# Kernel tuning notes

Measured on AMD Instinct MI355X. Metric: run time of the kernel, lower is better.

The kernel has to match this reference:

```python
import jax, jax.numpy as jnp
import numpy as np

SEQLEN = (512, 1024, 2048, 1536, 768, 1280, 896, 640)
HEAD_NUM = 16
HIDDEN = 1024  # head_size = 64


def setup_inputs() -> dict:
    key = jax.random.key(0)
    k1, k2 = jax.random.split(key)
    total_a = HEAD_NUM * sum(s * s for s in SEQLEN)  # packed per-seq (H, s, s) blocks
    a = jax.random.normal(k1, (total_a,), dtype=jnp.float32) * 0.02
    b = jax.random.normal(k2, (sum(SEQLEN), HIDDEN), dtype=jnp.float32)
    return {"a": a, "b": b, "seqlen": list(SEQLEN), "head_num": HEAD_NUM}


def reference(a, b, seqlen, head_num):
    """Ragged strided bmm2: per sequence i, per head h:
    C_i[:, h*hs:(h+1)*hs] = A_i[h] @ B_i[:, h*hs:(h+1)*hs].
    a packed flat as sum_i (head_num, s_i, s_i); b is (sum(s), hidden).
    """
    hidden = b.shape[1]
    hs = hidden // head_num
    outs = []
    a_off = 0
    t_off = 0
    for s in seqlen:  # static loop over ragged batch (lengths are compile-time)
        ai = jax.lax.dynamic_slice(a, (a_off,), (head_num * s * s,)).reshape(head_num, s, s)
        bi = jax.lax.dynamic_slice(b, (t_off, 0), (s, hidden)).reshape(s, head_num, hs)
        # (H, q, k) x (k, H, d) -> (q, H, d) -> (q, hidden)
        ci = jnp.einsum('hqk,khd->qhd', ai, bi).reshape(s, hidden)
        outs.append(ci)
        a_off += head_num * s * s
        t_off += s
    return jnp.concatenate(outs, axis=0)  # (sum(seqlen), hidden)
```

## Files before the change

### kernel.cpp

```cpp
#include <hip/hip_runtime.h>
#include <hip/hip_bf16.h>

typedef __attribute__((ext_vector_type(4))) float f32x4;
typedef __attribute__((ext_vector_type(8))) short bf16x8;

__device__ inline unsigned short f2b(float f) {
    union { float f; unsigned u; } v; v.f = f;
    unsigned r = v.u + 0x7FFF + ((v.u >> 16) & 1);
    return (unsigned short)(r >> 16);
}
__device__ inline unsigned pack2(float lo, float hi) {
    return (unsigned)f2b(lo) | ((unsigned)f2b(hi) << 16);
}

#define LDB 40

__global__ __launch_bounds__(256) void bmm2_kernel(const float* __restrict__ a,
                                                   const float* __restrict__ b,
                                                   float* __restrict__ out) {
    const int  cumblk[9] = {0,64,192,448,640,736,896,1008,1088};
    const int  slen[8]   = {512,1024,2048,1536,768,1280,896,640};
    const long aoff[8]   = {0,4194304,20971520,88080384,125829120,135266304,161480704,174325760};
    const int  toff[8]   = {0,512,1536,3584,5120,5888,7168,8064};

    __shared__ unsigned short Bt[64 * LDB];

    int bid = blockIdx.x;
    int i = 0;
    #pragma unroll
    for (int t = 0; t < 7; ++t) if (bid >= cumblk[t + 1]) i = t + 1;

    int rem  = bid - cumblk[i];
    int s    = slen[i];
    int nmb  = s >> 7;
    int head = rem / nmb;
    int mb   = rem - head * nmb;

    const float* A  = a + aoff[i] + (long)head * s * s + (long)mb * 128 * s;
    const float* Bp = b + (long)toff[i] * 1024 + head * 64;
    float*       Cp = out + (long)(toff[i] + mb * 128) * 1024 + head * 64;

    int tid  = threadIdx.x;
    int lane = tid & 63;
    int wave = tid >> 6;
    int lrow = lane & 15;
    int lgrp = lane >> 4;

    f32x4 acc[2][4] = {};

    int k2 = tid >> 4;
    int j0 = (tid & 15) * 4;

    const float* arow0 = A + (long)(wave * 32 + lrow) * s + lgrp * 8;
    const float* arow1 = arow0 + (long)16 * s;

    for (int k0 = 0; k0 < s; k0 += 32) {
        f32x4 a00 = *(const f32x4*)(arow0 + k0);
        f32x4 a01 = *(const f32x4*)(arow0 + k0 + 4);
        f32x4 a10 = *(const f32x4*)(arow1 + k0);
        f32x4 a11 = *(const f32x4*)(arow1 + k0 + 4);

        const float* bp = Bp + (long)(k0 + 2 * k2) * 1024 + j0;
        f32x4 b0 = *(const f32x4*)bp;
        f32x4 b1 = *(const f32x4*)(bp + 1024);

        __syncthreads();
        #pragma unroll
        for (int e = 0; e < 4; ++e)
            *(unsigned*)&Bt[(j0 + e) * LDB + 2 * k2] = pack2(b0[e], b1[e]);
        __syncthreads();

        bf16x8 bf[4];
        #pragma unroll
        for (int nt = 0; nt < 4; ++nt)
            bf[nt] = *(const bf16x8*)&Bt[(nt * 16 + lrow) * LDB + lgrp * 8];

        bf16x8 af0, af1;
        #pragma unroll
        for (int e = 0; e < 4; ++e) {
            af0[e]     = (short)f2b(a00[e]);
            af0[e + 4] = (short)f2b(a01[e]);
            af1[e]     = (short)f2b(a10[e]);
            af1[e + 4] = (short)f2b(a11[e]);
        }

        #pragma unroll
        for (int nt = 0; nt < 4; ++nt) {
            acc[0][nt] = __builtin_amdgcn_mfma_f32_16x16x32_bf16(af0, bf[nt], acc[0][nt], 0, 0, 0);
            acc[1][nt] = __builtin_amdgcn_mfma_f32_16x16x32_bf16(af1, bf[nt], acc[1][nt], 0, 0, 0);
        }
    }

    #pragma unroll
    for (int mt = 0; mt < 2; ++mt)
        #pragma unroll
        for (int nt = 0; nt < 4; ++nt)
            #pragma unroll
            for (int r = 0; r < 4; ++r) {
                int q = wave * 32 + mt * 16 + lgrp * 4 + r;
                Cp[(long)q * 1024 + nt * 16 + lrow] = acc[mt][nt][r];
            }
}

extern "C" void kernel_launch(void* const* d_in, const int* in_sizes, int n_in,
                              void* d_out, int out_size, void* d_ws, size_t ws_size,
                              hipStream_t stream) {
    const float* a = (const float*)d_in[0];
    const float* b = (const float*)d_in[1];
    float* out = (float*)d_out;
    bmm2_kernel<<<1088, 256, 0, stream>>>(a, b, out);
}
```

Measured before the change: 181.3 us.

## Pre-transpose B to bf16 in workspace and drop LDS staging in bmm2

```diff
diff --git a/kernel.cpp b/kernel.cpp
--- a/kernel.cpp
+++ b/kernel.cpp
@@ -4,90 +4,116 @@
 typedef __attribute__((ext_vector_type(4))) float f32x4;
 typedef __attribute__((ext_vector_type(8))) short bf16x8;
 
-__device__ inline unsigned short f2b(float f) {
+__device__ inline short f2b(float f) {
     union { float f; unsigned u; } v; v.f = f;
     unsigned r = v.u + 0x7FFF + ((v.u >> 16) & 1);
-    return (unsigned short)(r >> 16);
+    return (short)(r >> 16);
 }
 __device__ inline unsigned pack2(float lo, float hi) {
-    return (unsigned)f2b(lo) | ((unsigned)f2b(hi) << 16);
-}
-
-#define LDB 40
-
-__global__ __launch_bounds__(256) void bmm2_kernel(const float* __restrict__ a,
-                                                   const float* __restrict__ b,
-                                                   float* __restrict__ out) {
-    const int  cumblk[9] = {0,64,192,448,640,736,896,1008,1088};
-    const int  slen[8]   = {512,1024,2048,1536,768,1280,896,640};
-    const long aoff[8]   = {0,4194304,20971520,88080384,125829120,135266304,161480704,174325760};
-    const int  toff[8]   = {0,512,1536,3584,5120,5888,7168,8064};
-
-    __shared__ unsigned short Bt[64 * LDB];
+    return (unsigned)(unsigned short)f2b(lo) | ((unsigned)(unsigned short)f2b(hi) << 16);
+}
+
+__global__ __launch_bounds__(256) void transposeB(const float* __restrict__ b,
+                                                  unsigned short* __restrict__ bt) {
+    const int cumtb[9] = {0,128,384,896,1280,1472,1792,2016,2176};
+    const int slen[8]  = {512,1024,2048,1536,768,1280,896,640};
+    const int toff[8]  = {0,512,1536,3584,5120,5888,7168,8064};
+    __shared__ unsigned short T[64][72];
 
     int bid = blockIdx.x;
     int i = 0;
     #pragma unroll
+    for (int t = 0; t < 7; ++t) if (bid >= cumtb[t + 1]) i = t + 1;
+    int rem  = bid - cumtb[i];
+    int s    = slen[i];
+    int nkt  = s >> 6;
+    int head = rem / nkt;
+    int t0   = (rem - head * nkt) << 6;
+
+    int tid = threadIdx.x;
+    int row = tid >> 2, cg = tid & 3;
+    const float* src = b + (long)(toff[i] + t0 + row) * 1024 + head * 64 + cg * 16;
+    #pragma unroll
+    for (int e4 = 0; e4 < 4; ++e4) {
+        f32x4 v = *(const f32x4*)(src + e4 * 4);
+        #pragma unroll
+        for (int e = 0; e < 4; ++e)
+            T[cg * 16 + e4 * 4 + e][row] = (unsigned short)f2b(v[e]);
+    }
+    __syncthreads();
+    int col = tid >> 2, kq = tid & 3;
+    unsigned short* dst = bt + (long)toff[i] * 1024 + (long)head * 64 * s
+                             + (long)col * s + t0 + kq * 16;
+    *(bf16x8*)dst       = *(const bf16x8*)&T[col][kq * 16];
+    *(bf16x8*)(dst + 8) = *(const bf16x8*)&T[col][kq * 16 + 8];
+}
+
+__global__ __launch_bounds__(256) void bmm2_main(const float* __restrict__ a,
+                                                 const unsigned short* __restrict__ bt,
+                                                 float* __restrict__ out) {
+    const int  cumblk[9] = {0,256,448,608,736,848,944,1024,1088};
+    const int  slen[8]   = {2048,1536,1280,1024,896,768,640,512};
+    const long aoff[8]   = {20971520,88080384,135266304,4194304,161480704,125829120,174325760,0};
+    const int  toff[8]   = {1536,3584,5888,512,7168,5120,8064,0};
+
+    int bid = blockIdx.x;
+    int i = 0;
+    #pragma unroll
     for (int t = 0; t < 7; ++t) if (bid >= cumblk[t + 1]) i = t + 1;
-
     int rem  = bid - cumblk[i];
     int s    = slen[i];
     int nmb  = s >> 7;
     int head = rem / nmb;
     int mb   = rem - head * nmb;
 
-    const float* A  = a + aoff[i] + (long)head * s * s + (long)mb * 128 * s;
-    const float* Bp = b + (long)toff[i] * 1024 + head * 64;
-    float*       Cp = out + (long)(toff[i] + mb * 128) * 1024 + head * 64;
-
-    int tid  = threadIdx.x;
-    int lane = tid & 63;
-    int wave = tid >> 6;
-    int lrow = lane & 15;
-    int lgrp = lane >> 4;
+    const float* A = a + aoff[i] + (long)head * s * s + (long)mb * 128 * s;
+    const unsigned short* Bt = bt + (long)toff[i] * 1024 + (long)head * 64 * s;
+    float* Cp = out + (long)(toff[i] + mb * 128) * 1024 + head * 64;
+
+    int tid = threadIdx.x, lane = tid & 63, wave = tid >> 6;
+    int lrow = lane & 15, lgrp = lane >> 4;
+
+    const float* ar0 = A + (long)(wave * 32 + lrow) * s + lgrp * 8;
+    const float* ar1 = ar0 + (long)16 * s;
+    const unsigned short* bp = Bt + (long)lrow * s + lgrp * 8;
 
     f32x4 acc[2][4] = {};
 
-    int k2 = tid >> 4;
-    int j0 = (tid & 15) * 4;
-
-    const float* arow0 = A + (long)(wave * 32 + lrow) * s + lgrp * 8;
-    const float* arow1 = arow0 + (long)16 * s;
-
-    for (int k0 = 0; k0 < s; k0 += 32) {
-        f32x4 a00 = *(const f32x4*)(arow0 + k0);
-        f32x4 a01 = *(const f32x4*)(arow0 + k0 + 4);
-        f32x4 a10 = *(const f32x4*)(arow1 + k0);
-        f32x4 a11 = *(const f32x4*)(arow1 + k0 + 4);
-
-        const float* bp = Bp + (long)(k0 + 2 * k2) * 1024 + j0;
-        f32x4 b0 = *(const f32x4*)bp;
-        f32x4 b1 = *(const f32x4*)(bp + 1024);
-
-        __syncthreads();
-        #pragma unroll
-        for (int e = 0; e < 4; ++e)
-            *(unsigned*)&Bt[(j0 + e) * LDB + 2 * k2] = pack2(b0[e], b1[e]);
-        __syncthreads();
-
-        bf16x8 bf[4];
-        #pragma unroll
-        for (int nt = 0; nt < 4; ++nt)
-            bf[nt] = *(const bf16x8*)&Bt[(nt * 16 + lrow) * LDB + lgrp * 8];
-
-        bf16x8 af0, af1;
+    for (int k0 = 0; k0 < s; k0 += 64) {
+        f32x4 a00 = *(const f32x4*)(ar0 + k0);
+        f32x4 a01 = *(const f32x4*)(ar0 + k0 + 4);
+        f32x4 a10 = *(const f32x4*)(ar1 + k0);
+        f32x4 a11 = *(const f32x4*)(ar1 + k0 + 4);
+        f32x4 a02 = *(const f32x4*)(ar0 + k0 + 32);
+        f32x4 a03 = *(const f32x4*)(ar0 + k0 + 36);
+        f32x4 a12 = *(const f32x4*)(ar1 + k0 + 32);
+        f32x4 a13 = *(const f32x4*)(ar1 + k0 + 36);
+
+        bf16x8 bf0[4], bf1[4];
+        #pragma unroll
+        for (int nt = 0; nt < 4; ++nt) {
+            bf0[nt] = *(const bf16x8*)(bp + (long)nt * 16 * s + k0);
+            bf1[nt] = *(const bf16x8*)(bp + (long)nt * 16 * s + k0 + 32);
+        }
+
+        bf16x8 af0, af1, af2, af3;
         #pragma unroll
         for (int e = 0; e < 4; ++e) {
-            af0[e]     = (short)f2b(a00[e]);
-            af0[e + 4] = (short)f2b(a01[e]);
-            af1[e]     = (short)f2b(a10[e]);
-            af1[e + 4] = (short)f2b(a11[e]);
-        }
-
-        #pragma unroll
-        for (int nt = 0; nt < 4; ++nt) {
-            acc[0][nt] = __builtin_amdgcn_mfma_f32_16x16x32_bf16(af0, bf[nt], acc[0][nt], 0, 0, 0);
-            acc[1][nt] = __builtin_amdgcn_mfma_f32_16x16x32_bf16(af1, bf[nt], acc[1][nt], 0, 0, 0);
+            af0[e] = f2b(a00[e]); af0[e + 4] = f2b(a01[e]);
+            af1[e] = f2b(a10[e]); af1[e + 4] = f2b(a11[e]);
+            af2[e] = f2b(a02[e]); af2[e + 4] = f2b(a03[e]);
+            af3[e] = f2b(a12[e]); af3[e + 4] = f2b(a13[e]);
+        }
+
+        #pragma unroll
+        for (int nt = 0; nt < 4; ++nt) {
+            acc[0][nt] = __builtin_amdgcn_mfma_f32_16x16x32_bf16(af0, bf0[nt], acc[0][nt], 0, 0, 0);
+            acc[1][nt] = __builtin_amdgcn_mfma_f32_16x16x32_bf16(af1, bf0[nt], acc[1][nt], 0, 0, 0);
+        }
+        #pragma unroll
+        for (int nt = 0; nt < 4; ++nt) {
+            acc[0][nt] = __builtin_amdgcn_mfma_f32_16x16x32_bf16(af2, bf1[nt], acc[0][nt], 0, 0, 0);
+            acc[1][nt] = __builtin_amdgcn_mfma_f32_16x16x32_bf16(af3, bf1[nt], acc[1][nt], 0, 0, 0);
         }
     }
 
@@ -102,11 +128,89 @@
             }
 }
 
+#define LDB 40
+__global__ __launch_bounds__(256) void bmm2_kernel_lds(const float* __restrict__ a,
+                                                       const float* __restrict__ b,
+                                                       float* __restrict__ out) {
+    const int  cumblk[9] = {0,64,192,448,640,736,896,1008,1088};
+    const int  slen[8]   = {512,1024,2048,1536,768,1280,896,640};
+    const long aoff[8]   = {0,4194304,20971520,88080384,125829120,135266304,161480704,174325760};
+    const int  toff[8]   = {0,512,1536,3584,5120,5888,7168,8064};
+    __shared__ unsigned short Bt[64 * LDB];
+
+    int bid = blockIdx.x;
+    int i = 0;
+    #pragma unroll
+    for (int t = 0; t < 7; ++t) if (bid >= cumblk[t + 1]) i = t + 1;
+    int rem = bid - cumblk[i];
+    int s = slen[i];
+    int nmb = s >> 7;
+    int head = rem / nmb;
+    int mb = rem - head * nmb;
+
+    const float* A  = a + aoff[i] + (long)head * s * s + (long)mb * 128 * s;
+    const float* Bp = b + (long)toff[i] * 1024 + head * 64;
+    float*       Cp = out + (long)(toff[i] + mb * 128) * 1024 + head * 64;
+
+    int tid = threadIdx.x, lane = tid & 63, wave = tid >> 6;
+    int lrow = lane & 15, lgrp = lane >> 4;
+    f32x4 acc[2][4] = {};
+    int k2 = tid >> 4;
+    int j0 = (tid & 15) * 4;
+    const float* arow0 = A + (long)(wave * 32 + lrow) * s + lgrp * 8;
+    const float* arow1 = arow0 + (long)16 * s;
+
+    for (int k0 = 0; k0 < s; k0 += 32) {
+        f32x4 a00 = *(const f32x4*)(arow0 + k0);
+        f32x4 a01 = *(const f32x4*)(arow0 + k0 + 4);
+        f32x4 a10 = *(const f32x4*)(arow1 + k0);
+        f32x4 a11 = *(const f32x4*)(arow1 + k0 + 4);
+        const float* bpp = Bp + (long)(k0 + 2 * k2) * 1024 + j0;
+        f32x4 b0 = *(const f32x4*)bpp;
+        f32x4 b1 = *(const f32x4*)(bpp + 1024);
+        __syncthreads();
+        #pragma unroll
+        for (int e = 0; e < 4; ++e)
+            *(unsigned*)&Bt[(j0 + e) * LDB + 2 * k2] = pack2(b0[e], b1[e]);
+        __syncthreads();
+        bf16x8 bf[4];
+        #pragma unroll
+        for (int nt = 0; nt < 4; ++nt)
+            bf[nt] = *(const bf16x8*)&Bt[(nt * 16 + lrow) * LDB + lgrp * 8];
+        bf16x8 af0, af1;
+        #pragma unroll
+        for (int e = 0; e < 4; ++e) {
+            af0[e] = f2b(a00[e]); af0[e + 4] = f2b(a01[e]);
+            af1[e] = f2b(a10[e]); af1[e + 4] = f2b(a11[e]);
+        }
+        #pragma unroll
+        for (int nt = 0; nt < 4; ++nt) {
+            acc[0][nt] = __builtin_amdgcn_mfma_f32_16x16x32_bf16(af0, bf[nt], acc[0][nt], 0, 0, 0);
+            acc[1][nt] = __builtin_amdgcn_mfma_f32_16x16x32_bf16(af1, bf[nt], acc[1][nt], 0, 0, 0);
+        }
+    }
+    #pragma unroll
+    for (int mt = 0; mt < 2; ++mt)
+        #pragma unroll
+        for (int nt = 0; nt < 4; ++nt)
+            #pragma unroll
+            for (int r = 0; r < 4; ++r) {
+                int q = wave * 32 + mt * 16 + lgrp * 4 + r;
+                Cp[(long)q * 1024 + nt * 16 + lrow] = acc[mt][nt][r];
+            }
+}
+
 extern "C" void kernel_launch(void* const* d_in, const int* in_sizes, int n_in,
                               void* d_out, int out_size, void* d_ws, size_t ws_size,
                               hipStream_t stream) {
     const float* a = (const float*)d_in[0];
     const float* b = (const float*)d_in[1];
     float* out = (float*)d_out;
-    bmm2_kernel<<<1088, 256, 0, stream>>>(a, b, out);
-}
+    const size_t BT_BYTES = 8704UL * 1024UL * 2UL;
+    if (ws_size >= BT_BYTES) {
+        transposeB<<<2176, 256, 0, stream>>>(b, (unsigned short*)d_ws);
+        bmm2_main<<<1088, 256, 0, stream>>>(a, (const unsigned short*)d_ws, out);
+    } else {
+        bmm2_kernel_lds<<<1088, 256, 0, stream>>>(a, b, out);
+    }
+}
```

Result: slower. 228.9 us (+26.2%).

## Double-buffer B tile with 64-wide K steps, smaller blocks, longest-first scheduling

Applied to the files above, without the earlier changes.

```diff
diff --git a/kernel.cpp b/kernel.cpp
--- a/kernel.cpp
+++ b/kernel.cpp
@@ -4,101 +4,131 @@
 typedef __attribute__((ext_vector_type(4))) float f32x4;
 typedef __attribute__((ext_vector_type(8))) short bf16x8;
 
-__device__ inline unsigned short f2b(float f) {
-    union { float f; unsigned u; } v; v.f = f;
-    unsigned r = v.u + 0x7FFF + ((v.u >> 16) & 1);
-    return (unsigned short)(r >> 16);
+__device__ __forceinline__ unsigned cvt2(float lo, float hi) {
+    float2 t; t.x = lo; t.y = hi;
+    __hip_bfloat162 h = __float22bfloat162_rn(t);
+    union { __hip_bfloat162 h; unsigned u; } c; c.h = h; return c.u;
 }
-__device__ inline unsigned pack2(float lo, float hi) {
-    return (unsigned)f2b(lo) | ((unsigned)f2b(hi) << 16);
+__device__ __forceinline__ bf16x8 cvt8(f32x4 lo, f32x4 hi) {
+    union { bf16x8 v; unsigned u[4]; } r;
+    r.u[0] = cvt2(lo[0], lo[1]); r.u[1] = cvt2(lo[2], lo[3]);
+    r.u[2] = cvt2(hi[0], hi[1]); r.u[3] = cvt2(hi[2], hi[3]);
+    return r.v;
 }
 
-#define LDB 40
+__global__ __launch_bounds__(128, 4) void bmm2_k(const float* __restrict__ a,
+                                                 const float* __restrict__ b,
+                                                 float* __restrict__ out) {
+    const int  cumblk[9] = {0,512,896,1216,1472,1696,1888,2048,2176};
+    const int  slen[8]   = {2048,1536,1280,1024,896,768,640,512};
+    const long aoff[8]   = {20971520,88080384,135266304,4194304,161480704,125829120,174325760,0};
+    const int  toff[8]   = {1536,3584,5888,512,7168,5120,8064,0};
 
-__global__ __launch_bounds__(256) void bmm2_kernel(const float* __restrict__ a,
-                                                   const float* __restrict__ b,
-                                                   float* __restrict__ out) {
-    const int  cumblk[9] = {0,64,192,448,640,736,896,1008,1088};
-    const int  slen[8]   = {512,1024,2048,1536,768,1280,896,640};
-    const long aoff[8]   = {0,4194304,20971520,88080384,125829120,135266304,161480704,174325760};
-    const int  toff[8]   = {0,512,1536,3584,5120,5888,7168,8064};
-
-    __shared__ unsigned short Bt[64 * LDB];
+    __shared__ unsigned short Bt[2][64 * 72];
 
     int bid = blockIdx.x;
     int i = 0;
     #pragma unroll
     for (int t = 0; t < 7; ++t) if (bid >= cumblk[t + 1]) i = t + 1;
-
     int rem  = bid - cumblk[i];
     int s    = slen[i];
-    int nmb  = s >> 7;
+    int nmb  = s >> 6;
     int head = rem / nmb;
     int mb   = rem - head * nmb;
 
-    const float* A  = a + aoff[i] + (long)head * s * s + (long)mb * 128 * s;
+    const float* A  = a + aoff[i] + (long)head * s * s + (long)mb * 64 * s;
     const float* Bp = b + (long)toff[i] * 1024 + head * 64;
-    float*       Cp = out + (long)(toff[i] + mb * 128) * 1024 + head * 64;
+    float*       Cp = out + (long)(toff[i] + mb * 64) * 1024 + head * 64;
 
-    int tid  = threadIdx.x;
-    int lane = tid & 63;
-    int wave = tid >> 6;
-    int lrow = lane & 15;
-    int lgrp = lane >> 4;
+    int tid = threadIdx.x, lane = tid & 63, wave = tid >> 6;
+    int lrow = lane & 15, lgrp = lane >> 4;
+
+    int j0 = (tid & 15) * 4;
+    int kb = (tid >> 4) * 8;
+    const float* bsrc = Bp + (long)kb * 1024 + j0;
+
+    const float* ar0 = A + (long)(wave * 32 + lrow) * s + lgrp * 8;
+    const float* ar1 = ar0 + (long)16 * s;
 
     f32x4 acc[2][4] = {};
+    int NT = s >> 6;
 
-    int k2 = tid >> 4;
-    int j0 = (tid & 15) * 4;
+    {
+        f32x4 r[8];
+        #pragma unroll
+        for (int q = 0; q < 8; ++q) r[q] = *(const f32x4*)(bsrc + (long)q * 1024);
+        #pragma unroll
+        for (int e = 0; e < 4; ++e) {
+            uint4 w;
+            w.x = cvt2(r[0][e], r[1][e]); w.y = cvt2(r[2][e], r[3][e]);
+            w.z = cvt2(r[4][e], r[5][e]); w.w = cvt2(r[6][e], r[7][e]);
+            *(uint4*)&Bt[0][(j0 + e) * 72 + kb] = w;
+        }
+    }
+    __syncthreads();
 
-    const float* arow0 = A + (long)(wave * 32 + lrow) * s + lgrp * 8;
-    const float* arow1 = arow0 + (long)16 * s;
+    for (int t = 0; t < NT; ++t) {
+        int cur = t & 1, nxt = cur ^ 1;
+        int k0 = t << 6;
+        int kn = (t + 1 < NT) ? (k0 + 64) : 0;
 
-    for (int k0 = 0; k0 < s; k0 += 32) {
-        f32x4 a00 = *(const f32x4*)(arow0 + k0);
-        f32x4 a01 = *(const f32x4*)(arow0 + k0 + 4);
-        f32x4 a10 = *(const f32x4*)(arow1 + k0);
-        f32x4 a11 = *(const f32x4*)(arow1 + k0 + 4);
-
-        const float* bp = Bp + (long)(k0 + 2 * k2) * 1024 + j0;
-        f32x4 b0 = *(const f32x4*)bp;
-        f32x4 b1 = *(const f32x4*)(bp + 1024);
+        f32x4 r[8];
+        #pragma unroll
+        for (int q = 0; q < 8; ++q) r[q] = *(const f32x4*)(bsrc + (long)(kn + q) * 1024);
 
         __syncthreads();
-        #pragma unroll
-        for (int e = 0; e < 4; ++e)
-            *(unsigned*)&Bt[(j0 + e) * LDB + 2 * k2] = pack2(b0[e], b1[e]);
-        __syncthreads();
 
-        bf16x8 bf[4];
-        #pragma unroll
-        for (int nt = 0; nt < 4; ++nt)
-            bf[nt] = *(const bf16x8*)&Bt[(nt * 16 + lrow) * LDB + lgrp * 8];
-
-        bf16x8 af0, af1;
         #pragma unroll
         for (int e = 0; e < 4; ++e) {
-            af0[e]     = (short)f2b(a00[e]);
-            af0[e + 4] = (short)f2b(a01[e]);
-            af1[e]     = (short)f2b(a10[e]);
-            af1[e + 4] = (short)f2b(a11[e]);
+            uint4 w;
+            w.x = cvt2(r[0][e], r[1][e]); w.y = cvt2(r[2][e], r[3][e]);
+            w.z = cvt2(r[4][e], r[5][e]); w.w = cvt2(r[6][e], r[7][e]);
+            *(uint4*)&Bt[nxt][(j0 + e) * 72 + kb] = w;
         }
 
-        #pragma unroll
-        for (int nt = 0; nt < 4; ++nt) {
-            acc[0][nt] = __builtin_amdgcn_mfma_f32_16x16x32_bf16(af0, bf[nt], acc[0][nt], 0, 0, 0);
-            acc[1][nt] = __builtin_amdgcn_mfma_f32_16x16x32_bf16(af1, bf[nt], acc[1][nt], 0, 0, 0);
+        f32x4 a000 = *(const f32x4*)(ar0 + k0);
+        f32x4 a001 = *(const f32x4*)(ar0 + k0 + 4);
+        f32x4 a010 = *(const f32x4*)(ar0 + k0 + 32);
+        f32x4 a011 = *(const f32x4*)(ar0 + k0 + 36);
+        f32x4 a100 = *(const f32x4*)(ar1 + k0);
+        f32x4 a101 = *(const f32x4*)(ar1 + k0 + 4);
+        f32x4 a110 = *(const f32x4*)(ar1 + k0 + 32);
+        f32x4 a111 = *(const f32x4*)(ar1 + k0 + 36);
+
+        {
+            bf16x8 af0 = cvt8(a000, a001), af1 = cvt8(a100, a101);
+            bf16x8 bf[4];
+            #pragma unroll
+            for (int n = 0; n < 4; ++n)
+                bf[n] = *(const bf16x8*)&Bt[cur][(n * 16 + lrow) * 72 + lgrp * 8];
+            #pragma unroll
+            for (int n = 0; n < 4; ++n) {
+                acc[0][n] = __builtin_amdgcn_mfma_f32_16x16x32_bf16(af0, bf[n], acc[0][n], 0, 0, 0);
+                acc[1][n] = __builtin_amdgcn_mfma_f32_16x16x32_bf16(af1, bf[n], acc[1][n], 0, 0, 0);
+            }
+        }
+        {
+            bf16x8 af2 = cvt8(a010, a011), af3 = cvt8(a110, a111);
+            bf16x8 bf[4];
+            #pragma unroll
+            for (int n = 0; n < 4; ++n)
+                bf[n] = *(const bf16x8*)&Bt[cur][(n * 16 + lrow) * 72 + 32 + lgrp * 8];
+            #pragma unroll
+            for (int n = 0; n < 4; ++n) {
+                acc[0][n] = __builtin_amdgcn_mfma_f32_16x16x32_bf16(af2, bf[n], acc[0][n], 0, 0, 0);
+                acc[1][n] = __builtin_amdgcn_mfma_f32_16x16x32_bf16(af3, bf[n], acc[1][n], 0, 0, 0);
+            }
         }
     }
 
     #pragma unroll
     for (int mt = 0; mt < 2; ++mt)
         #pragma unroll
-        for (int nt = 0; nt < 4; ++nt)
+        for (int n = 0; n < 4; ++n)
             #pragma unroll
-            for (int r = 0; r < 4; ++r) {
-                int q = wave * 32 + mt * 16 + lgrp * 4 + r;
-                Cp[(long)q * 1024 + nt * 16 + lrow] = acc[mt][nt][r];
+            for (int rr = 0; rr < 4; ++rr) {
+                int q = wave * 32 + mt * 16 + lgrp * 4 + rr;
+                Cp[(long)q * 1024 + n * 16 + lrow] = acc[mt][n][rr];
             }
 }
 
@@ -108,5 +138,5 @@
     const float* a = (const float*)d_in[0];
     const float* b = (const float*)d_in[1];
     float* out = (float*)d_out;
-    bmm2_kernel<<<1088, 256, 0, stream>>>(a, b, out);
+    bmm2_k<<<2176, 128, 0, stream>>>(a, b, out);
 }
```

Measured after the change: 191.6 us. 1.06x slower.
